# Optimization experiments

Measured on AMD Instinct MI355X. Metric: run time of the kernel, lower is better.

The kernel has to match this reference:

```python
import jax, jax.numpy as jnp
import numpy as np

N_NODES = 50000


def _gin_conv(x, src, dst, w1, b1, w2, b2):
    # sum-aggregate neighbor features: agg[i] = sum_{(j->i) in E} x[j]
    agg = jax.ops.segment_sum(x[src], dst, num_segments=N_NODES)
    h = x + agg  # eps = 0 (PyG GINConv default, not trainable)
    h = jnp.maximum(h @ w1 + b1, 0.0) @ w2 + b2
    return h


def setup_inputs() -> dict:
    key = jax.random.key(0)
    ks = jax.random.split(key, 10)
    d_in, d_h, d_out = 128, 256, 2
    E = 600000
    x = jax.random.normal(ks[0], (N_NODES, d_in), dtype=jnp.float32)
    edge_index = jax.random.randint(ks[1], (2, E), 0, N_NODES, dtype=jnp.int64)
    s = lambda k, sh: jax.random.normal(k, sh, dtype=jnp.float32) * (1.0 / np.sqrt(sh[0]))
    return {
        "x": x,
        "edge_index": edge_index,
        "w1": s(ks[2], (d_in, d_h)), "b1": jnp.zeros((d_h,), jnp.float32),
        "w2": s(ks[3], (d_h, d_h)), "b2": jnp.zeros((d_h,), jnp.float32),
        "w3": s(ks[4], (d_h, d_h)), "b3": jnp.zeros((d_h,), jnp.float32),
        "w4": s(ks[5], (d_h, d_out)), "b4": jnp.zeros((d_out,), jnp.float32),
    }


def reference(x, edge_index, w1, b1, w2, b2, w3, b3, w4, b4):
    src, dst = edge_index[0], edge_index[1]
    h = _gin_conv(x, src, dst, w1, b1, w2, b2)
    h = jnp.maximum(h, 0.0)  # F.relu between the two GINConv layers
    h = _gin_conv(h, src, dst, w3, b3, w4, b4)
    return jax.nn.log_softmax(h, axis=1)
```

## Files before the change

### kernel.cpp

```cpp
#include <hip/hip_runtime.h>
#include <hip/hip_bf16.h>


typedef __attribute__((ext_vector_type(8))) short bf16x8;
typedef __attribute__((ext_vector_type(4))) float f32x4;

static __device__ __forceinline__ unsigned short f2bf(float f) {
    unsigned int u = __float_as_uint(f);
    unsigned int r = (u + 0x7fffu + ((u >> 16) & 1u)) >> 16;
    return (unsigned short)r;
}
static __device__ __forceinline__ float bf2f(unsigned short s) {
    return __uint_as_float(((unsigned int)s) << 16);
}
static __device__ __forceinline__ float bflo(unsigned int u) {
    return __uint_as_float(u << 16);
}
static __device__ __forceinline__ float bfhi(unsigned int u) {
    return __uint_as_float(u & 0xffff0000u);
}

#define S1 136
#define S2 264

__global__ __launch_bounds__(256) void prep_kernel(
    const float* __restrict__ x, short* __restrict__ x_bf,
    const float* __restrict__ w1, const float* __restrict__ w2, const float* __restrict__ w3,
    short* __restrict__ w1t, short* __restrict__ w2t, short* __restrict__ w3t,
    int* __restrict__ deg, int M, int zB, int cB)
{
    const int b = blockIdx.x;
    const int t = threadIdx.x;
    if (b < zB) {
        const int idx = b * 1024 + t * 4;
        if (idx + 3 < M) {
            *(int4*)(deg + idx) = make_int4(0, 0, 0, 0);
        } else {
            #pragma unroll
            for (int i = 0; i < 4; ++i) if (idx + i < M) deg[idx + i] = 0;
        }
        return;
    }
    if (b < zB + cB) {
        const int i = (b - zB) * 256 + t;
        const int n4 = M * 32;
        if (i >= n4) return;
        const float4 v = *(const float4*)(x + (size_t)i * 4);
        ushort4 o;
        o.x = f2bf(v.x); o.y = f2bf(v.y); o.z = f2bf(v.z); o.w = f2bf(v.w);
        *(ushort4*)(x_bf + (size_t)i * 4) = o;
        return;
    }
    const int tb = b - zB - cB;
    const int z = tb >> 6;
    const int rem = tb & 63;
    const int kb = rem & 7;
    const int nb = rem >> 3;
    const float* in; short* outb; int K, ostride;
    if (z == 0)      { in = w1; outb = w1t; K = 128; ostride = S1; }
    else if (z == 1) { in = w2; outb = w2t; K = 256; ostride = S2; }
    else             { in = w3; outb = w3t; K = 256; ostride = S2; }
    const int N = 256;
    const int k0 = kb * 32;
    if (k0 >= K) return;
    const int n0 = nb * 32;
    __shared__ float tile[32][33];
    const int tx = t & 31;
    const int ty = t >> 5;
    #pragma unroll
    for (int i = 0; i < 4; ++i)
        tile[ty + 8 * i][tx] = in[(size_t)(k0 + ty + 8 * i) * N + n0 + tx];
    __syncthreads();
    #pragma unroll
    for (int i = 0; i < 4; ++i)
        outb[(size_t)(n0 + ty + 8 * i) * ostride + k0 + tx] = (short)f2bf(tile[tx][ty + 8 * i]);
}

__global__ __launch_bounds__(256) void degree_kernel(
    const int* __restrict__ dst, int* __restrict__ deg, int E)
{
    const int e = blockIdx.x * 256 + threadIdx.x;
    if (e < E) atomicAdd(&deg[dst[e]], 1);
}

__global__ __launch_bounds__(256) void block_sum_kernel(
    const int* __restrict__ deg, int* __restrict__ bsum, int M)
{
    const int b = blockIdx.x, t = threadIdx.x;
    const int idx = b * 1024 + t * 4;
    int s = 0;
    if (idx + 3 < M) {
        const int4 v = *(const int4*)(deg + idx);
        s = v.x + v.y + v.z + v.w;
    } else {
        #pragma unroll
        for (int i = 0; i < 4; ++i) if (idx + i < M) s += deg[idx + i];
    }
    #pragma unroll
    for (int off = 32; off > 0; off >>= 1) s += __shfl_down(s, off);
    __shared__ int ws[4];
    if ((t & 63) == 0) ws[t >> 6] = s;
    __syncthreads();
    if (t == 0) bsum[b] = ws[0] + ws[1] + ws[2] + ws[3];
}

__global__ __launch_bounds__(256) void scan_blocks2_kernel(
    const int* __restrict__ deg, const int* __restrict__ bsum,
    int* __restrict__ rowptr, int* __restrict__ cur, int M, int E, int nB)
{
    const int b = blockIdx.x, t = threadIdx.x;
    __shared__ int sboff;
    if (t < 64) {
        const int v = (t < nB) ? bsum[t] : 0;
        int inc = v;
        #pragma unroll
        for (int off = 1; off < 64; off <<= 1) {
            const int u = __shfl_up(inc, off);
            if (t >= off) inc += u;
        }
        const int prev = __shfl(inc, (b == 0) ? 0 : (b - 1));
        if (t == 0) sboff = (b == 0) ? 0 : prev;
    }
    const int idx = b * 1024 + t * 4;
    int4 d = make_int4(0, 0, 0, 0);
    if (idx + 3 < M) {
        d = *(const int4*)(deg + idx);
    } else {
        if (idx + 0 < M) d.x = deg[idx + 0];
        if (idx + 1 < M) d.y = deg[idx + 1];
        if (idx + 2 < M) d.z = deg[idx + 2];
        if (idx + 3 < M) d.w = deg[idx + 3];
    }
    const int tot = d.x + d.y + d.z + d.w;
    const int lane = t & 63, wid = t >> 6;
    int inc = tot;
    #pragma unroll
    for (int off = 1; off < 64; off <<= 1) {
        const int u = __shfl_up(inc, off);
        if (lane >= off) inc += u;
    }
    __shared__ int wsum[4];
    if (lane == 63) wsum[wid] = inc;
    __syncthreads();
    int woff = 0;
    #pragma unroll
    for (int w = 0; w < 4; ++w) if (w < wid) woff += wsum[w];
    int p = sboff + woff + (inc - tot);
    if (idx + 0 < M) { rowptr[idx + 0] = p; cur[idx + 0] = p; } p += d.x;
    if (idx + 1 < M) { rowptr[idx + 1] = p; cur[idx + 1] = p; } p += d.y;
    if (idx + 2 < M) { rowptr[idx + 2] = p; cur[idx + 2] = p; } p += d.z;
    if (idx + 3 < M) { rowptr[idx + 3] = p; cur[idx + 3] = p; }
    if (b == 0 && t == 0) rowptr[M] = E;
}

__global__ __launch_bounds__(256) void fill_kernel(
    const int* __restrict__ src, const int* __restrict__ dst,
    int* __restrict__ cur, int* __restrict__ srcs, int E)
{
    const int e = blockIdx.x * 256 + threadIdx.x;
    if (e >= E) return;
    const int p = atomicAdd(&cur[dst[e]], 1);
    srcs[p] = src[e];
}

__global__ __launch_bounds__(256) void gather_add_d128(
    const short* __restrict__ feat,
    const int* __restrict__ rowptr, const int* __restrict__ srcs,
    short* __restrict__ outb, int M)
{
    const int row = blockIdx.x * 4 + (threadIdx.x >> 6);
    if (row >= M) return;
    const int lane = threadIdx.x & 63;
    const int half = lane >> 5;
    const int o = (lane & 31) * 4;
    float a0 = 0.f, a1 = 0.f, a2 = 0.f, a3 = 0.f;
    if (half == 0) {
        const uint2 u = *(const uint2*)(feat + (size_t)row * 128 + o);
        a0 = bflo(u.x); a1 = bfhi(u.x); a2 = bflo(u.y); a3 = bfhi(u.y);
    }
    const int jb = rowptr[row], je = rowptr[row + 1];
    int j = jb;
    for (; j + 8 <= je; j += 8) {
        uint2 v[4];
        #pragma unroll
        for (int t = 0; t < 4; ++t) {
            const int s = srcs[j + 2 * t + half];
            v[t] = *(const uint2*)(feat + (size_t)s * 128 + o);
        }
        #pragma unroll
        for (int t = 0; t < 4; ++t) {
            a0 += bflo(v[t].x); a1 += bfhi(v[t].x);
            a2 += bflo(v[t].y); a3 += bfhi(v[t].y);
        }
    }
    for (; j + 2 <= je; j += 2) {
        const int s = srcs[j + half];
        const uint2 v = *(const uint2*)(feat + (size_t)s * 128 + o);
        a0 += bflo(v.x); a1 += bfhi(v.x); a2 += bflo(v.y); a3 += bfhi(v.y);
    }
    if (j < je && half == 0) {
        const uint2 v = *(const uint2*)(feat + (size_t)srcs[j] * 128 + o);
        a0 += bflo(v.x); a1 += bfhi(v.x); a2 += bflo(v.y); a3 += bfhi(v.y);
    }
    a0 += __shfl_down(a0, 32);
    a1 += __shfl_down(a1, 32);
    a2 += __shfl_down(a2, 32);
    a3 += __shfl_down(a3, 32);
    if (half == 0) {
        uint2 up;
        up.x = (unsigned int)f2bf(a0) | ((unsigned int)f2bf(a1) << 16);
        up.y = (unsigned int)f2bf(a2) | ((unsigned int)f2bf(a3) << 16);
        *(uint2*)(outb + (size_t)row * S1 + o) = up;
    }
}

__global__ __launch_bounds__(256) void gather_add_d256(
    const short* __restrict__ feat,
    const int* __restrict__ rowptr, const int* __restrict__ srcs,
    short* __restrict__ outb, int M)
{
    const int row = blockIdx.x * 4 + (threadIdx.x >> 6);
    if (row >= M) return;
    const int lane = threadIdx.x & 63;
    const int half = lane >> 5;
    const int o = (lane & 31) * 8;
    float a[8];
    #pragma unroll
    for (int k = 0; k < 8; ++k) a[k] = 0.f;
    if (half == 0) {
        const uint4 u = *(const uint4*)(feat + (size_t)row * 256 + o);
        a[0] = bflo(u.x); a[1] = bfhi(u.x); a[2] = bflo(u.y); a[3] = bfhi(u.y);
        a[4] = bflo(u.z); a[5] = bfhi(u.z); a[6] = bflo(u.w); a[7] = bfhi(u.w);
    }
    const int jb = rowptr[row], je = rowptr[row + 1];
    int j = jb;
    for (; j + 8 <= je; j += 8) {
        uint4 v[4];
        #pragma unroll
        for (int t = 0; t < 4; ++t) {
            const int s = srcs[j + 2 * t + half];
            v[t] = *(const uint4*)(feat + (size_t)s * 256 + o);
        }
        #pragma unroll
        for (int t = 0; t < 4; ++t) {
            a[0] += bflo(v[t].x); a[1] += bfhi(v[t].x);
            a[2] += bflo(v[t].y); a[3] += bfhi(v[t].y);
            a[4] += bflo(v[t].z); a[5] += bfhi(v[t].z);
            a[6] += bflo(v[t].w); a[7] += bfhi(v[t].w);
        }
    }
    for (; j + 2 <= je; j += 2) {
        const int s = srcs[j + half];
        const uint4 v = *(const uint4*)(feat + (size_t)s * 256 + o);
        a[0] += bflo(v.x); a[1] += bfhi(v.x); a[2] += bflo(v.y); a[3] += bfhi(v.y);
        a[4] += bflo(v.z); a[5] += bfhi(v.z); a[6] += bflo(v.w); a[7] += bfhi(v.w);
    }
    if (j < je && half == 0) {
        const uint4 v = *(const uint4*)(feat + (size_t)srcs[j] * 256 + o);
        a[0] += bflo(v.x); a[1] += bfhi(v.x); a[2] += bflo(v.y); a[3] += bfhi(v.y);
        a[4] += bflo(v.z); a[5] += bfhi(v.z); a[6] += bflo(v.w); a[7] += bfhi(v.w);
    }
    #pragma unroll
    for (int k = 0; k < 8; ++k) a[k] += __shfl_down(a[k], 32);
    if (half == 0) {
        uint4 up;
        up.x = (unsigned int)f2bf(a[0]) | ((unsigned int)f2bf(a[1]) << 16);
        up.y = (unsigned int)f2bf(a[2]) | ((unsigned int)f2bf(a[3]) << 16);
        up.z = (unsigned int)f2bf(a[4]) | ((unsigned int)f2bf(a[5]) << 16);
        up.w = (unsigned int)f2bf(a[6]) | ((unsigned int)f2bf(a[7]) << 16);
        *(uint4*)(outb + (size_t)row * S2 + o) = up;
    }
}

__global__ __launch_bounds__(256) void layer1_fused(
    const short* __restrict__ h1in,
    const short* __restrict__ w1t,
    const float* __restrict__ b1,
    const short* __restrict__ w2t,
    const float* __restrict__ b2,
    short* __restrict__ h1,
    int M)
{
    __shared__ short sT[64 * S2];
    const int tid  = threadIdx.x;
    const int lane = tid & 63;
    const int wid  = tid >> 6;
    const int r16  = lane & 15;
    const int q    = lane >> 4;
    const int tm   = blockIdx.x * 64;
    const int wn   = wid * 64;

    f32x4 acc[4][4];
    #pragma unroll
    for (int i = 0; i < 4; ++i)
        #pragma unroll
        for (int j = 0; j < 4; ++j)
            acc[i][j] = (f32x4)0.f;

    const short* Abase = h1in + (size_t)tm * S1;
    #pragma unroll
    for (int k0 = 0; k0 < 128; k0 += 32) {
        bf16x8 af[4], bfr[4];
        #pragma unroll
        for (int i = 0; i < 4; ++i)
            af[i] = *(const bf16x8*)(Abase + (size_t)(i * 16 + r16) * S1 + k0 + q * 8);
        #pragma unroll
        for (int j = 0; j < 4; ++j)
            bfr[j] = *(const bf16x8*)(w1t + (size_t)(wn + j * 16 + r16) * S1 + k0 + q * 8);
        #pragma unroll
        for (int i = 0; i < 4; ++i)
            #pragma unroll
            for (int j = 0; j < 4; ++j)
                acc[i][j] = __builtin_amdgcn_mfma_f32_16x16x32_bf16(af[i], bfr[j], acc[i][j], 0, 0, 0);
    }

    #pragma unroll
    for (int j = 0; j < 4; ++j) {
        const int col = wn + j * 16 + r16;
        const float bj = b1[col];
        #pragma unroll
        for (int i = 0; i < 4; ++i)
            #pragma unroll
            for (int r = 0; r < 4; ++r) {
                float v = fmaxf(acc[i][j][r] + bj, 0.f);
                sT[(i * 16 + q * 4 + r) * S2 + col] = (short)f2bf(v);
            }
    }
    __syncthreads();

    #pragma unroll
    for (int i = 0; i < 4; ++i)
        #pragma unroll
        for (int j = 0; j < 4; ++j)
            acc[i][j] = (f32x4)0.f;

    #pragma unroll
    for (int k0 = 0; k0 < 256; k0 += 32) {
        bf16x8 af[4], bfr[4];
        #pragma unroll
        for (int i = 0; i < 4; ++i)
            af[i] = *(const bf16x8*)(&sT[(i * 16 + r16) * S2 + k0 + q * 8]);
        #pragma unroll
        for (int j = 0; j < 4; ++j)
            bfr[j] = *(const bf16x8*)(w2t + (size_t)(wn + j * 16 + r16) * S2 + k0 + q * 8);
        #pragma unroll
        for (int i = 0; i < 4; ++i)
            #pragma unroll
            for (int j = 0; j < 4; ++j)
                acc[i][j] = __builtin_amdgcn_mfma_f32_16x16x32_bf16(af[i], bfr[j], acc[i][j], 0, 0, 0);
    }
    __syncthreads();

    #pragma unroll
    for (int j = 0; j < 4; ++j) {
        const int col = wn + j * 16 + r16;
        const float bj = b2[col];
        #pragma unroll
        for (int i = 0; i < 4; ++i)
            #pragma unroll
            for (int r = 0; r < 4; ++r) {
                float v = fmaxf(acc[i][j][r] + bj, 0.f);
                sT[(i * 16 + q * 4 + r) * S2 + col] = (short)f2bf(v);
            }
    }
    __syncthreads();

    #pragma unroll
    for (int c = 0; c < 8; ++c) {
        const int idx = tid + c * 256;
        const int row = idx >> 5;
        const int ch  = idx & 31;
        const int rg  = tm + row;
        if (rg < M) {
            const uint4 v = *(const uint4*)(&sT[row * S2 + ch * 8]);
            *(uint4*)(h1 + (size_t)rg * 256 + ch * 8) = v;
        }
    }
}

__global__ __launch_bounds__(256) void layer2_fused(
    const short* __restrict__ h2in,
    const short* __restrict__ w3t,
    const float* __restrict__ b3,
    const float* __restrict__ w4,
    const float* __restrict__ b4,
    float* __restrict__ out,
    int M)
{
    __shared__ short sT[64 * S2];
    const int tid  = threadIdx.x;
    const int lane = tid & 63;
    const int wid  = tid >> 6;
    const int r16  = lane & 15;
    const int q    = lane >> 4;
    const int tm   = blockIdx.x * 64;
    const int wn   = wid * 64;

    f32x4 acc[4][4];
    #pragma unroll
    for (int i = 0; i < 4; ++i)
        #pragma unroll
        for (int j = 0; j < 4; ++j)
            acc[i][j] = (f32x4)0.f;

    const short* Abase = h2in + (size_t)tm * S2;
    #pragma unroll
    for (int k0 = 0; k0 < 256; k0 += 32) {
        bf16x8 af[4], bfr[4];
        #pragma unroll
        for (int i = 0; i < 4; ++i)
            af[i] = *(const bf16x8*)(Abase + (size_t)(i * 16 + r16) * S2 + k0 + q * 8);
        #pragma unroll
        for (int j = 0; j < 4; ++j)
            bfr[j] = *(const bf16x8*)(w3t + (size_t)(wn + j * 16 + r16) * S2 + k0 + q * 8);
        #pragma unroll
        for (int i = 0; i < 4; ++i)
            #pragma unroll
            for (int j = 0; j < 4; ++j)
                acc[i][j] = __builtin_amdgcn_mfma_f32_16x16x32_bf16(af[i], bfr[j], acc[i][j], 0, 0, 0);
    }

    #pragma unroll
    for (int j = 0; j < 4; ++j) {
        const int col = wn + j * 16 + r16;
        const float bj = b3[col];
        #pragma unroll
        for (int i = 0; i < 4; ++i)
            #pragma unroll
            for (int r = 0; r < 4; ++r) {
                float v = fmaxf(acc[i][j][r] + bj, 0.f);
                sT[(i * 16 + q * 4 + r) * S2 + col] = (short)f2bf(v);
            }
    }
    __syncthreads();

    const int row = tid >> 2;
    const int qd  = tid & 3;
    const short* tp = &sT[row * S2 + qd * 64];
    const float* w4p = w4 + qd * 128;
    float s0 = 0.f, s1 = 0.f;
    #pragma unroll 8
    for (int k = 0; k < 64; ++k) {
        const float a = bf2f((unsigned short)tp[k]);
        const float2 w = *(const float2*)(w4p + 2 * k);
        s0 = fmaf(a, w.x, s0);
        s1 = fmaf(a, w.y, s1);
    }
    s0 += __shfl_down(s0, 2, 4);  s1 += __shfl_down(s1, 2, 4);
    s0 += __shfl_down(s0, 1, 4);  s1 += __shfl_down(s1, 1, 4);
    if (qd == 0) {
        const int rg = tm + row;
        if (rg < M) {
            s0 += b4[0];
            s1 += b4[1];
            const float m = fmaxf(s0, s1);
            const float l = logf(__expf(s0 - m) + __expf(s1 - m));
            float2 o;
            o.x = s0 - m - l;
            o.y = s1 - m - l;
            *(float2*)(out + (size_t)rg * 2) = o;
        }
    }
}

extern "C" void kernel_launch(void* const* d_in, const int* in_sizes, int n_in,
                              void* d_out, int out_size, void* d_ws, size_t ws_size,
                              hipStream_t stream)
{
    const float* x  = (const float*)d_in[0];
    const int*   ei = (const int*)d_in[1];
    const float* w1 = (const float*)d_in[2];
    const float* b1 = (const float*)d_in[3];
    const float* w2 = (const float*)d_in[4];
    const float* b2 = (const float*)d_in[5];
    const float* w3 = (const float*)d_in[6];
    const float* b3 = (const float*)d_in[7];
    const float* w4 = (const float*)d_in[8];
    const float* b4 = (const float*)d_in[9];

    const int DIN = 128, DH = 256;
    const int M = in_sizes[0] / DIN;
    const int E = in_sizes[1] / 2;
    const int* src = ei;
    const int* dst = ei + E;
    const int nB = (M + 1023) / 1024;

    int* deg    = (int*)d_ws;
    int* cur    = deg + M;
    int* rowptr = cur + M;
    int* bsum   = rowptr + (M + 1);
    int* srcs   = bsum + 64;
    size_t off = ((size_t)(3 * M + 1 + 64 + E) * sizeof(int) + 255) & ~(size_t)255;
    short* x_bf = (short*)((char*)d_ws + off);  off += (size_t)M * DIN * 2;
    off = (off + 255) & ~(size_t)255;
    short* h1in = (short*)((char*)d_ws + off);  off += (size_t)M * S1 * 2;
    off = (off + 255) & ~(size_t)255;
    short* h1   = (short*)((char*)d_ws + off);  off += (size_t)M * DH * 2;
    off = (off + 255) & ~(size_t)255;
    short* h2in = (short*)((char*)d_ws + off);  off += (size_t)M * S2 * 2;
    off = (off + 255) & ~(size_t)255;
    short* w1t  = (short*)((char*)d_ws + off);  off += (size_t)DH * S1 * 2;
    off = (off + 255) & ~(size_t)255;
    short* w2t  = (short*)((char*)d_ws + off);  off += (size_t)DH * S2 * 2;
    off = (off + 255) & ~(size_t)255;
    short* w3t  = (short*)((char*)d_ws + off);  off += (size_t)DH * S2 * 2;

    const int zB = nB;
    const int cB = (M * 32 + 255) / 256;
    prep_kernel<<<zB + cB + 192, 256, 0, stream>>>(
        x, x_bf, w1, w2, w3, w1t, w2t, w3t, deg, M, zB, cB);

    degree_kernel<<<(E + 255) / 256, 256, 0, stream>>>(dst, deg, E);
    block_sum_kernel<<<nB, 256, 0, stream>>>(deg, bsum, M);
    scan_blocks2_kernel<<<nB, 256, 0, stream>>>(deg, bsum, rowptr, cur, M, E, nB);
    fill_kernel<<<(E + 255) / 256, 256, 0, stream>>>(src, dst, cur, srcs, E);

    const int nblk = (M + 63) / 64;

    gather_add_d128<<<(M + 3) / 4, 256, 0, stream>>>(x_bf, rowptr, srcs, h1in, M);
    layer1_fused<<<nblk, 256, 0, stream>>>(h1in, w1t, b1, w2t, b2, h1, M);

    gather_add_d256<<<(M + 3) / 4, 256, 0, stream>>>(h1, rowptr, srcs, h2in, M);
    layer2_fused<<<nblk, 256, 0, stream>>>(h2in, w3t, b3, w4, b4, (float*)d_out, M);
}
```

Before: 285.1 us.

## Fuse neighbor gather-aggregation into MLP kernels and merge degree counting into prep

Each GIN layer's sum-aggregation now writes its result straight into shared memory inside the MLP kernel, with the row tile shrunk to 32 rows. This removes the global h1in/h2in intermediates and two kernel launches. The degree atomics move into the prep kernel, and degree zeroing becomes a hipMemsetAsync. The cost is that each block runs its gather serially, 8 rows per wave, and MFMA work per block is smaller, so latency hiding in the gather and weight reuse in the GEMM may get worse.

```diff
diff --git a/kernel.cpp b/kernel.cpp
--- a/kernel.cpp
+++ b/kernel.cpp
@@ -22,27 +22,19 @@
 
 #define S1 136
 #define S2 264
+#define TM 32
 
 __global__ __launch_bounds__(256) void prep_kernel(
     const float* __restrict__ x, short* __restrict__ x_bf,
     const float* __restrict__ w1, const float* __restrict__ w2, const float* __restrict__ w3,
     short* __restrict__ w1t, short* __restrict__ w2t, short* __restrict__ w3t,
-    int* __restrict__ deg, int M, int zB, int cB)
+    const int* __restrict__ dst, int* __restrict__ deg,
+    int M, int E, int cB)
 {
     const int b = blockIdx.x;
     const int t = threadIdx.x;
-    if (b < zB) {
-        const int idx = b * 1024 + t * 4;
-        if (idx + 3 < M) {
-            *(int4*)(deg + idx) = make_int4(0, 0, 0, 0);
-        } else {
-            #pragma unroll
-            for (int i = 0; i < 4; ++i) if (idx + i < M) deg[idx + i] = 0;
-        }
-        return;
-    }
-    if (b < zB + cB) {
-        const int i = (b - zB) * 256 + t;
+    if (b < cB) {
+        const int i = b * 256 + t;
         const int n4 = M * 32;
         if (i >= n4) return;
         const float4 v = *(const float4*)(x + (size_t)i * 4);
@@ -51,35 +43,33 @@
         *(ushort4*)(x_bf + (size_t)i * 4) = o;
         return;
     }
-    const int tb = b - zB - cB;
-    const int z = tb >> 6;
-    const int rem = tb & 63;
-    const int kb = rem & 7;
-    const int nb = rem >> 3;
-    const float* in; short* outb; int K, ostride;
-    if (z == 0)      { in = w1; outb = w1t; K = 128; ostride = S1; }
-    else if (z == 1) { in = w2; outb = w2t; K = 256; ostride = S2; }
-    else             { in = w3; outb = w3t; K = 256; ostride = S2; }
-    const int N = 256;
-    const int k0 = kb * 32;
-    if (k0 >= K) return;
-    const int n0 = nb * 32;
-    __shared__ float tile[32][33];
-    const int tx = t & 31;
-    const int ty = t >> 5;
-    #pragma unroll
-    for (int i = 0; i < 4; ++i)
-        tile[ty + 8 * i][tx] = in[(size_t)(k0 + ty + 8 * i) * N + n0 + tx];
-    __syncthreads();
-    #pragma unroll
-    for (int i = 0; i < 4; ++i)
-        outb[(size_t)(n0 + ty + 8 * i) * ostride + k0 + tx] = (short)f2bf(tile[tx][ty + 8 * i]);
-}
-
-__global__ __launch_bounds__(256) void degree_kernel(
-    const int* __restrict__ dst, int* __restrict__ deg, int E)
-{
-    const int e = blockIdx.x * 256 + threadIdx.x;
+    if (b < cB + 192) {
+        const int tb = b - cB;
+        const int z = tb >> 6;
+        const int rem = tb & 63;
+        const int kb = rem & 7;
+        const int nb = rem >> 3;
+        const float* in; short* outb; int K, ostride;
+        if (z == 0)      { in = w1; outb = w1t; K = 128; ostride = S1; }
+        else if (z == 1) { in = w2; outb = w2t; K = 256; ostride = S2; }
+        else             { in = w3; outb = w3t; K = 256; ostride = S2; }
+        const int N = 256;
+        const int k0 = kb * 32;
+        if (k0 >= K) return;
+        const int n0 = nb * 32;
+        __shared__ float tile[32][33];
+        const int tx = t & 31;
+        const int ty = t >> 5;
+        #pragma unroll
+        for (int i = 0; i < 4; ++i)
+            tile[ty + 8 * i][tx] = in[(size_t)(k0 + ty + 8 * i) * N + n0 + tx];
+        __syncthreads();
+        #pragma unroll
+        for (int i = 0; i < 4; ++i)
+            outb[(size_t)(n0 + ty + 8 * i) * ostride + k0 + tx] = (short)f2bf(tile[tx][ty + 8 * i]);
+        return;
+    }
+    const int e = (b - cB - 192) * 256 + t;
     if (e < E) atomicAdd(&deg[dst[e]], 1);
 }
 
@@ -163,117 +153,9 @@
     srcs[p] = src[e];
 }
 
-__global__ __launch_bounds__(256) void gather_add_d128(
-    const short* __restrict__ feat,
+__global__ __launch_bounds__(256) void fused_layer1(
+    const short* __restrict__ x_bf,
     const int* __restrict__ rowptr, const int* __restrict__ srcs,
-    short* __restrict__ outb, int M)
-{
-    const int row = blockIdx.x * 4 + (threadIdx.x >> 6);
-    if (row >= M) return;
-    const int lane = threadIdx.x & 63;
-    const int half = lane >> 5;
-    const int o = (lane & 31) * 4;
-    float a0 = 0.f, a1 = 0.f, a2 = 0.f, a3 = 0.f;
-    if (half == 0) {
-        const uint2 u = *(const uint2*)(feat + (size_t)row * 128 + o);
-        a0 = bflo(u.x); a1 = bfhi(u.x); a2 = bflo(u.y); a3 = bfhi(u.y);
-    }
-    const int jb = rowptr[row], je = rowptr[row + 1];
-    int j = jb;
-    for (; j + 8 <= je; j += 8) {
-        uint2 v[4];
-        #pragma unroll
-        for (int t = 0; t < 4; ++t) {
-            const int s = srcs[j + 2 * t + half];
-            v[t] = *(const uint2*)(feat + (size_t)s * 128 + o);
-        }
-        #pragma unroll
-        for (int t = 0; t < 4; ++t) {
-            a0 += bflo(v[t].x); a1 += bfhi(v[t].x);
-            a2 += bflo(v[t].y); a3 += bfhi(v[t].y);
-        }
-    }
-    for (; j + 2 <= je; j += 2) {
-        const int s = srcs[j + half];
-        const uint2 v = *(const uint2*)(feat + (size_t)s * 128 + o);
-        a0 += bflo(v.x); a1 += bfhi(v.x); a2 += bflo(v.y); a3 += bfhi(v.y);
-    }
-    if (j < je && half == 0) {
-        const uint2 v = *(const uint2*)(feat + (size_t)srcs[j] * 128 + o);
-        a0 += bflo(v.x); a1 += bfhi(v.x); a2 += bflo(v.y); a3 += bfhi(v.y);
-    }
-    a0 += __shfl_down(a0, 32);
-    a1 += __shfl_down(a1, 32);
-    a2 += __shfl_down(a2, 32);
-    a3 += __shfl_down(a3, 32);
-    if (half == 0) {
-        uint2 up;
-        up.x = (unsigned int)f2bf(a0) | ((unsigned int)f2bf(a1) << 16);
-        up.y = (unsigned int)f2bf(a2) | ((unsigned int)f2bf(a3) << 16);
-        *(uint2*)(outb + (size_t)row * S1 + o) = up;
-    }
-}
-
-__global__ __launch_bounds__(256) void gather_add_d256(
-    const short* __restrict__ feat,
-    const int* __restrict__ rowptr, const int* __restrict__ srcs,
-    short* __restrict__ outb, int M)
-{
-    const int row = blockIdx.x * 4 + (threadIdx.x >> 6);
-    if (row >= M) return;
-    const int lane = threadIdx.x & 63;
-    const int half = lane >> 5;
-    const int o = (lane & 31) * 8;
-    float a[8];
-    #pragma unroll
-    for (int k = 0; k < 8; ++k) a[k] = 0.f;
-    if (half == 0) {
-        const uint4 u = *(const uint4*)(feat + (size_t)row * 256 + o);
-        a[0] = bflo(u.x); a[1] = bfhi(u.x); a[2] = bflo(u.y); a[3] = bfhi(u.y);
-        a[4] = bflo(u.z); a[5] = bfhi(u.z); a[6] = bflo(u.w); a[7] = bfhi(u.w);
-    }
-    const int jb = rowptr[row], je = rowptr[row + 1];
-    int j = jb;
-    for (; j + 8 <= je; j += 8) {
-        uint4 v[4];
-        #pragma unroll
-        for (int t = 0; t < 4; ++t) {
-            const int s = srcs[j + 2 * t + half];
-            v[t] = *(const uint4*)(feat + (size_t)s * 256 + o);
-        }
-        #pragma unroll
-        for (int t = 0; t < 4; ++t) {
-            a[0] += bflo(v[t].x); a[1] += bfhi(v[t].x);
-            a[2] += bflo(v[t].y); a[3] += bfhi(v[t].y);
-            a[4] += bflo(v[t].z); a[5] += bfhi(v[t].z);
-            a[6] += bflo(v[t].w); a[7] += bfhi(v[t].w);
-        }
-    }
-    for (; j + 2 <= je; j += 2) {
-        const int s = srcs[j + half];
-        const uint4 v = *(const uint4*)(feat + (size_t)s * 256 + o);
-        a[0] += bflo(v.x); a[1] += bfhi(v.x); a[2] += bflo(v.y); a[3] += bfhi(v.y);
-        a[4] += bflo(v.z); a[5] += bfhi(v.z); a[6] += bflo(v.w); a[7] += bfhi(v.w);
-    }
-    if (j < je && half == 0) {
-        const uint4 v = *(const uint4*)(feat + (size_t)srcs[j] * 256 + o);
-        a[0] += bflo(v.x); a[1] += bfhi(v.x); a[2] += bflo(v.y); a[3] += bfhi(v.y);
-        a[4] += bflo(v.z); a[5] += bfhi(v.z); a[6] += bflo(v.w); a[7] += bfhi(v.w);
-    }
-    #pragma unroll
-    for (int k = 0; k < 8; ++k) a[k] += __shfl_down(a[k], 32);
-    if (half == 0) {
-        uint4 up;
-        up.x = (unsigned int)f2bf(a[0]) | ((unsigned int)f2bf(a[1]) << 16);
-        up.y = (unsigned int)f2bf(a[2]) | ((unsigned int)f2bf(a[3]) << 16);
-        up.z = (unsigned int)f2bf(a[4]) | ((unsigned int)f2bf(a[5]) << 16);
-        up.w = (unsigned int)f2bf(a[6]) | ((unsigned int)f2bf(a[7]) << 16);
-        *(uint4*)(outb + (size_t)row * S2 + o) = up;
-    }
-}
-
-__global__ __launch_bounds__(256) void layer1_fused(
-    const short* __restrict__ h1in,
     const short* __restrict__ w1t,
     const float* __restrict__ b1,
     const short* __restrict__ w2t,
@@ -281,70 +163,120 @@
     short* __restrict__ h1,
     int M)
 {
-    __shared__ short sT[64 * S2];
+    __shared__ short sBuf[TM * S2];
     const int tid  = threadIdx.x;
     const int lane = tid & 63;
     const int wid  = tid >> 6;
     const int r16  = lane & 15;
     const int q    = lane >> 4;
-    const int tm   = blockIdx.x * 64;
+    const int tm   = blockIdx.x * TM;
     const int wn   = wid * 64;
 
-    f32x4 acc[4][4];
-    #pragma unroll
-    for (int i = 0; i < 4; ++i)
+    {
+        const int half = lane >> 5;
+        const int o = (lane & 31) * 4;
+        for (int rr = 0; rr < 8; ++rr) {
+            const int r = wid * 8 + rr;
+            const int rg = tm + r;
+            if (rg >= M) break;
+            float a0 = 0.f, a1 = 0.f, a2 = 0.f, a3 = 0.f;
+            if (half == 0) {
+                const uint2 u = *(const uint2*)(x_bf + (size_t)rg * 128 + o);
+                a0 = bflo(u.x); a1 = bfhi(u.x); a2 = bflo(u.y); a3 = bfhi(u.y);
+            }
+            const int jb = rowptr[rg], je = rowptr[rg + 1];
+            int j = jb;
+            for (; j + 8 <= je; j += 8) {
+                uint2 v[4];
+                #pragma unroll
+                for (int t2 = 0; t2 < 4; ++t2) {
+                    const int s = srcs[j + 2 * t2 + half];
+                    v[t2] = *(const uint2*)(x_bf + (size_t)s * 128 + o);
+                }
+                #pragma unroll
+                for (int t2 = 0; t2 < 4; ++t2) {
+                    a0 += bflo(v[t2].x); a1 += bfhi(v[t2].x);
+                    a2 += bflo(v[t2].y); a3 += bfhi(v[t2].y);
+                }
+            }
+            for (; j + 2 <= je; j += 2) {
+                const int s = srcs[j + half];
+                const uint2 v = *(const uint2*)(x_bf + (size_t)s * 128 + o);
+                a0 += bflo(v.x); a1 += bfhi(v.x); a2 += bflo(v.y); a3 += bfhi(v.y);
+            }
+            if (j < je && half == 0) {
+                const uint2 v = *(const uint2*)(x_bf + (size_t)srcs[j] * 128 + o);
+                a0 += bflo(v.x); a1 += bfhi(v.x); a2 += bflo(v.y); a3 += bfhi(v.y);
+            }
+            a0 += __shfl_down(a0, 32);
+            a1 += __shfl_down(a1, 32);
+            a2 += __shfl_down(a2, 32);
+            a3 += __shfl_down(a3, 32);
+            if (half == 0) {
+                uint2 up;
+                up.x = (unsigned int)f2bf(a0) | ((unsigned int)f2bf(a1) << 16);
+                up.y = (unsigned int)f2bf(a2) | ((unsigned int)f2bf(a3) << 16);
+                *(uint2*)(&sBuf[r * S1 + o]) = up;
+            }
+        }
+    }
+    __syncthreads();
+
+    f32x4 acc[2][4];
+    #pragma unroll
+    for (int i = 0; i < 2; ++i)
         #pragma unroll
         for (int j = 0; j < 4; ++j)
             acc[i][j] = (f32x4)0.f;
 
-    const short* Abase = h1in + (size_t)tm * S1;
     #pragma unroll
     for (int k0 = 0; k0 < 128; k0 += 32) {
-        bf16x8 af[4], bfr[4];
-        #pragma unroll
-        for (int i = 0; i < 4; ++i)
-            af[i] = *(const bf16x8*)(Abase + (size_t)(i * 16 + r16) * S1 + k0 + q * 8);
+        bf16x8 af[2], bfr[4];
+        #pragma unroll
+        for (int i = 0; i < 2; ++i)
+            af[i] = *(const bf16x8*)(&sBuf[(i * 16 + r16) * S1 + k0 + q * 8]);
         #pragma unroll
         for (int j = 0; j < 4; ++j)
             bfr[j] = *(const bf16x8*)(w1t + (size_t)(wn + j * 16 + r16) * S1 + k0 + q * 8);
         #pragma unroll
-        for (int i = 0; i < 4; ++i)
+        for (int i = 0; i < 2; ++i)
             #pragma unroll
             for (int j = 0; j < 4; ++j)
                 acc[i][j] = __builtin_amdgcn_mfma_f32_16x16x32_bf16(af[i], bfr[j], acc[i][j], 0, 0, 0);
     }
+    __syncthreads();
 
     #pragma unroll
     for (int j = 0; j < 4; ++j) {
         const int col = wn + j * 16 + r16;
         const float bj = b1[col];
         #pragma unroll
-        for (int i = 0; i < 4; ++i)
+        for (int i = 0; i < 2; ++i)
             #pragma unroll
             for (int r = 0; r < 4; ++r) {
                 float v = fmaxf(acc[i][j][r] + bj, 0.f);
-                sT[(i * 16 + q * 4 + r) * S2 + col] = (short)f2bf(v);
-            }
-    }
-    __syncthreads();
-
-    #pragma unroll
-    for (int i = 0; i < 4; ++i)
+                sBuf[(i * 16 + q * 4 + r) * S2 + col] = (short)f2bf(v);
+            }
+    }
+    __syncthreads();
+
+    #pragma unroll
+    for (int i = 0; i < 2; ++i)
         #pragma unroll
         for (int j = 0; j < 4; ++j)
             acc[i][j] = (f32x4)0.f;
 
     #pragma unroll
     for (int k0 = 0; k0 < 256; k0 += 32) {
-        bf16x8 af[4], bfr[4];
-        #pragma unroll
-        for (int i = 0; i < 4; ++i)
-            af[i] = *(const bf16x8*)(&sT[(i * 16 + r16) * S2 + k0 + q * 8]);
+        bf16x8 af[2], bfr[4];
+        #pragma unroll
+        for (int i = 0; i < 2; ++i)
+            af[i] = *(const bf16x8*)(&sBuf[(i * 16 + r16) * S2 + k0 + q * 8]);
         #pragma unroll
         for (int j = 0; j < 4; ++j)
             bfr[j] = *(const bf16x8*)(w2t + (size_t)(wn + j * 16 + r16) * S2 + k0 + q * 8);
         #pragma unroll
-        for (int i = 0; i < 4; ++i)
+        for (int i = 0; i < 2; ++i)
             #pragma unroll
             for (int j = 0; j < 4; ++j)
                 acc[i][j] = __builtin_amdgcn_mfma_f32_16x16x32_bf16(af[i], bfr[j], acc[i][j], 0, 0, 0);
@@ -356,30 +288,31 @@
         const int col = wn + j * 16 + r16;
         const float bj = b2[col];
         #pragma unroll
-        for (int i = 0; i < 4; ++i)
+        for (int i = 0; i < 2; ++i)
             #pragma unroll
             for (int r = 0; r < 4; ++r) {
                 float v = fmaxf(acc[i][j][r] + bj, 0.f);
-                sT[(i * 16 + q * 4 + r) * S2 + col] = (short)f2bf(v);
-            }
-    }
-    __syncthreads();
-
-    #pragma unroll
-    for (int c = 0; c < 8; ++c) {
+                sBuf[(i * 16 + q * 4 + r) * S2 + col] = (short)f2bf(v);
+            }
+    }
+    __syncthreads();
+
+    #pragma unroll
+    for (int c = 0; c < 4; ++c) {
         const int idx = tid + c * 256;
         const int row = idx >> 5;
         const int ch  = idx & 31;
         const int rg  = tm + row;
         if (rg < M) {
-            const uint4 v = *(const uint4*)(&sT[row * S2 + ch * 8]);
+            const uint4 v = *(const uint4*)(&sBuf[row * S2 + ch * 8]);
             *(uint4*)(h1 + (size_t)rg * 256 + ch * 8) = v;
         }
     }
 }
 
-__global__ __launch_bounds__(256) void layer2_fused(
-    const short* __restrict__ h2in,
+__global__ __launch_bounds__(256) void fused_layer2(
+    const short* __restrict__ h1,
+    const int* __restrict__ rowptr, const int* __restrict__ srcs,
     const short* __restrict__ w3t,
     const float* __restrict__ b3,
     const float* __restrict__ w4,
@@ -387,67 +320,125 @@
     float* __restrict__ out,
     int M)
 {
-    __shared__ short sT[64 * S2];
+    __shared__ short sBuf[TM * S2];
     const int tid  = threadIdx.x;
     const int lane = tid & 63;
     const int wid  = tid >> 6;
     const int r16  = lane & 15;
     const int q    = lane >> 4;
-    const int tm   = blockIdx.x * 64;
+    const int tm   = blockIdx.x * TM;
     const int wn   = wid * 64;
 
-    f32x4 acc[4][4];
-    #pragma unroll
-    for (int i = 0; i < 4; ++i)
+    {
+        const int half = lane >> 5;
+        const int o = (lane & 31) * 8;
+        for (int rr = 0; rr < 8; ++rr) {
+            const int r = wid * 8 + rr;
+            const int rg = tm + r;
+            if (rg >= M) break;
+            float a[8];
+            #pragma unroll
+            for (int k = 0; k < 8; ++k) a[k] = 0.f;
+            if (half == 0) {
+                const uint4 u = *(const uint4*)(h1 + (size_t)rg * 256 + o);
+                a[0] = bflo(u.x); a[1] = bfhi(u.x); a[2] = bflo(u.y); a[3] = bfhi(u.y);
+                a[4] = bflo(u.z); a[5] = bfhi(u.z); a[6] = bflo(u.w); a[7] = bfhi(u.w);
+            }
+            const int jb = rowptr[rg], je = rowptr[rg + 1];
+            int j = jb;
+            for (; j + 8 <= je; j += 8) {
+                uint4 v[4];
+                #pragma unroll
+                for (int t2 = 0; t2 < 4; ++t2) {
+                    const int s = srcs[j + 2 * t2 + half];
+                    v[t2] = *(const uint4*)(h1 + (size_t)s * 256 + o);
+                }
+                #pragma unroll
+                for (int t2 = 0; t2 < 4; ++t2) {
+                    a[0] += bflo(v[t2].x); a[1] += bfhi(v[t2].x);
+                    a[2] += bflo(v[t2].y); a[3] += bfhi(v[t2].y);
+                    a[4] += bflo(v[t2].z); a[5] += bfhi(v[t2].z);
+                    a[6] += bflo(v[t2].w); a[7] += bfhi(v[t2].w);
+                }
+            }
+            for (; j + 2 <= je; j += 2) {
+                const int s = srcs[j + half];
+                const uint4 v = *(const uint4*)(h1 + (size_t)s * 256 + o);
+                a[0] += bflo(v.x); a[1] += bfhi(v.x); a[2] += bflo(v.y); a[3] += bfhi(v.y);
+                a[4] += bflo(v.z); a[5] += bfhi(v.z); a[6] += bflo(v.w); a[7] += bfhi(v.w);
+            }
+            if (j < je && half == 0) {
+                const uint4 v = *(const uint4*)(h1 + (size_t)srcs[j] * 256 + o);
+                a[0] += bflo(v.x); a[1] += bfhi(v.x); a[2] += bflo(v.y); a[3] += bfhi(v.y);
+                a[4] += bflo(v.z); a[5] += bfhi(v.z); a[6] += bflo(v.w); a[7] += bfhi(v.w);
+            }
+            #pragma unroll
+            for (int k = 0; k < 8; ++k) a[k] += __shfl_down(a[k], 32);
+            if (half == 0) {
+                uint4 up;
+                up.x = (unsigned int)f2bf(a[0]) | ((unsigned int)f2bf(a[1]) << 16);
+                up.y = (unsigned int)f2bf(a[2]) | ((unsigned int)f2bf(a[3]) << 16);
+                up.z = (unsigned int)f2bf(a[4]) | ((unsigned int)f2bf(a[5]) << 16);
+                up.w = (unsigned int)f2bf(a[6]) | ((unsigned int)f2bf(a[7]) << 16);
+                *(uint4*)(&sBuf[r * S2 + o]) = up;
+            }
+        }
+    }
+    __syncthreads();
+
+    f32x4 acc[2][4];
+    #pragma unroll
+    for (int i = 0; i < 2; ++i)
         #pragma unroll
         for (int j = 0; j < 4; ++j)
             acc[i][j] = (f32x4)0.f;
 
-    const short* Abase = h2in + (size_t)tm * S2;
     #pragma unroll
     for (int k0 = 0; k0 < 256; k0 += 32) {
-        bf16x8 af[4], bfr[4];
-        #pragma unroll
-        for (int i = 0; i < 4; ++i)
-            af[i] = *(const bf16x8*)(Abase + (size_t)(i * 16 + r16) * S2 + k0 + q * 8);
+        bf16x8 af[2], bfr[4];
+        #pragma unroll
+        for (int i = 0; i < 2; ++i)
+            af[i] = *(const bf16x8*)(&sBuf[(i * 16 + r16) * S2 + k0 + q * 8]);
         #pragma unroll
         for (int j = 0; j < 4; ++j)
             bfr[j] = *(const bf16x8*)(w3t + (size_t)(wn + j * 16 + r16) * S2 + k0 + q * 8);
         #pragma unroll
-        for (int i = 0; i < 4; ++i)
+        for (int i = 0; i < 2; ++i)
             #pragma unroll
             for (int j = 0; j < 4; ++j)
                 acc[i][j] = __builtin_amdgcn_mfma_f32_16x16x32_bf16(af[i], bfr[j], acc[i][j], 0, 0, 0);
     }
+    __syncthreads();
 
     #pragma unroll
     for (int j = 0; j < 4; ++j) {
         const int col = wn + j * 16 + r16;
         const float bj = b3[col];
         #pragma unroll
-        for (int i = 0; i < 4; ++i)
+        for (int i = 0; i < 2; ++i)
             #pragma unroll
             for (int r = 0; r < 4; ++r) {
                 float v = fmaxf(acc[i][j][r] + bj, 0.f);
-                sT[(i * 16 + q * 4 + r) * S2 + col] = (short)f2bf(v);
-            }
-    }
-    __syncthreads();
-
-    const int row = tid >> 2;
-    const int qd  = tid & 3;
-    const short* tp = &sT[row * S2 + qd * 64];
-    const float* w4p = w4 + qd * 128;
+                sBuf[(i * 16 + q * 4 + r) * S2 + col] = (short)f2bf(v);
+            }
+    }
+    __syncthreads();
+
+    const int row = tid >> 3;
+    const int qd  = tid & 7;
+    const short* tp = &sBuf[row * S2 + qd * 32];
+    const float* w4p = w4 + qd * 64;
     float s0 = 0.f, s1 = 0.f;
     #pragma unroll 8
-    for (int k = 0; k < 64; ++k) {
+    for (int k = 0; k < 32; ++k) {
         const float a = bf2f((unsigned short)tp[k]);
         const float2 w = *(const float2*)(w4p + 2 * k);
         s0 = fmaf(a, w.x, s0);
         s1 = fmaf(a, w.y, s1);
     }
-    s0 += __shfl_down(s0, 2, 4);  s1 += __shfl_down(s1, 2, 4);
-    s0 += __shfl_down(s0, 1, 4);  s1 += __shfl_down(s1, 1, 4);
+    s0 += __shfl_down(s0, 4, 8);  s1 += __shfl_down(s1, 4, 8);
+    s0 += __shfl_down(s0, 2, 8);  s1 += __shfl_down(s1, 2, 8);
+    s0 += __shfl_down(s0, 1, 8);  s1 += __shfl_down(s1, 1, 8);
     if (qd == 0) {
         const int rg = tm + row;
         if (rg < M) {
@@ -493,11 +484,7 @@
     size_t off = ((size_t)(3 * M + 1 + 64 + E) * sizeof(int) + 255) & ~(size_t)255;
     short* x_bf = (short*)((char*)d_ws + off);  off += (size_t)M * DIN * 2;
     off = (off + 255) & ~(size_t)255;
-    short* h1in = (short*)((char*)d_ws + off);  off += (size_t)M * S1 * 2;
-    off = (off + 255) & ~(size_t)255;
     short* h1   = (short*)((char*)d_ws + off);  off += (size_t)M * DH * 2;
-    off = (off + 255) & ~(size_t)255;
-    short* h2in = (short*)((char*)d_ws + off);  off += (size_t)M * S2 * 2;
     off = (off + 255) & ~(size_t)255;
     short* w1t  = (short*)((char*)d_ws + off);  off += (size_t)DH * S1 * 2;
     off = (off + 255) & ~(size_t)255;
@@ -505,21 +492,18 @@
     off = (off + 255) & ~(size_t)255;
     short* w3t  = (short*)((char*)d_ws + off);  off += (size_t)DH * S2 * 2;
 
-    const int zB = nB;
+    hipMemsetAsync(deg, 0, (size_t)M * sizeof(int), stream);
     const int cB = (M * 32 + 255) / 256;
-    prep_kernel<<<zB + cB + 192, 256, 0, stream>>>(
-        x, x_bf, w1, w2, w3, w1t, w2t, w3t, deg, M, zB, cB);
-
-    degree_kernel<<<(E + 255) / 256, 256, 0, stream>>>(dst, deg, E);
+    const int dB = (E + 255) / 256;
+    prep_kernel<<<cB + 192 + dB, 256, 0, stream>>>(
+        x, x_bf, w1, w2, w3, w1t, w2t, w3t, dst, deg, M, E, cB);
+
     block_sum_kernel<<<nB, 256, 0, stream>>>(deg, bsum, M);
     scan_blocks2_kernel<<<nB, 256, 0, stream>>>(deg, bsum, rowptr, cur, M, E, nB);
-    fill_kernel<<<(E + 255) / 256, 256, 0, stream>>>(src, dst, cur, srcs, E);
-
-    const int nblk = (M + 63) / 64;
-
-    gather_add_d128<<<(M + 3) / 4, 256, 0, stream>>>(x_bf, rowptr, srcs, h1in, M);
-    layer1_fused<<<nblk, 256, 0, stream>>>(h1in, w1t, b1, w2t, b2, h1, M);
-
-    gather_add_d256<<<(M + 3) / 4, 256, 0, stream>>>(h1, rowptr, srcs, h2in, M);
-    layer2_fused<<<nblk, 256, 0, stream>>>(h2in, w3t, b3, w4, b4, (float*)d_out, M);
-}
+    fill_kernel<<<dB, 256, 0, stream>>>(src, dst, cur, srcs, E);
+
+    const int nblk = (M + TM - 1) / TM;
+
+    fused_layer1<<<nblk, 256, 0, stream>>>(x_bf, rowptr, srcs, w1t, b1, w2t, b2, h1, M);
+    fused_layer2<<<nblk, 256, 0, stream>>>(h1, rowptr, srcs, w3t, b3, w4, b4, (float*)d_out, M);
+}
```

Measured after the change: 319.0 us. 1.12x slower.

## Fuse degree counting and block sums into prep kernel; widen d128 gather loads

Applied to the files above, without the earlier changes.

Zeroing of the degree and block-sum arrays moves to a hipMemsetAsync, and the degree atomics now run inside the prep kernel alongside the bf16 conversion and weight transposes. Each edge also atomically bumps its 1024-node block sum, which removes the separate degree and block_sum launches. The d128 gather now uses 16-byte loads, with four edge quarters per wave reduced by two shuffles. The cost is a second atomic per edge, which contends on only about 49 block counters.

```diff
diff --git a/kernel.cpp b/kernel.cpp
--- a/kernel.cpp
+++ b/kernel.cpp
@@ -27,22 +27,13 @@
     const float* __restrict__ x, short* __restrict__ x_bf,
     const float* __restrict__ w1, const float* __restrict__ w2, const float* __restrict__ w3,
     short* __restrict__ w1t, short* __restrict__ w2t, short* __restrict__ w3t,
-    int* __restrict__ deg, int M, int zB, int cB)
+    const int* __restrict__ dst, int* __restrict__ deg, int* __restrict__ bsum,
+    int M, int E, int cB)
 {
     const int b = blockIdx.x;
     const int t = threadIdx.x;
-    if (b < zB) {
-        const int idx = b * 1024 + t * 4;
-        if (idx + 3 < M) {
-            *(int4*)(deg + idx) = make_int4(0, 0, 0, 0);
-        } else {
-            #pragma unroll
-            for (int i = 0; i < 4; ++i) if (idx + i < M) deg[idx + i] = 0;
-        }
-        return;
-    }
-    if (b < zB + cB) {
-        const int i = (b - zB) * 256 + t;
+    if (b < cB) {
+        const int i = b * 256 + t;
         const int n4 = M * 32;
         if (i >= n4) return;
         const float4 v = *(const float4*)(x + (size_t)i * 4);
@@ -51,57 +42,38 @@
         *(ushort4*)(x_bf + (size_t)i * 4) = o;
         return;
     }
-    const int tb = b - zB - cB;
-    const int z = tb >> 6;
-    const int rem = tb & 63;
-    const int kb = rem & 7;
-    const int nb = rem >> 3;
-    const float* in; short* outb; int K, ostride;
-    if (z == 0)      { in = w1; outb = w1t; K = 128; ostride = S1; }
-    else if (z == 1) { in = w2; outb = w2t; K = 256; ostride = S2; }
-    else             { in = w3; outb = w3t; K = 256; ostride = S2; }
-    const int N = 256;
-    const int k0 = kb * 32;
-    if (k0 >= K) return;
-    const int n0 = nb * 32;
-    __shared__ float tile[32][33];
-    const int tx = t & 31;
-    const int ty = t >> 5;
-    #pragma unroll
-    for (int i = 0; i < 4; ++i)
-        tile[ty + 8 * i][tx] = in[(size_t)(k0 + ty + 8 * i) * N + n0 + tx];
-    __syncthreads();
-    #pragma unroll
-    for (int i = 0; i < 4; ++i)
-        outb[(size_t)(n0 + ty + 8 * i) * ostride + k0 + tx] = (short)f2bf(tile[tx][ty + 8 * i]);
-}
-
-__global__ __launch_bounds__(256) void degree_kernel(
-    const int* __restrict__ dst, int* __restrict__ deg, int E)
-{
-    const int e = blockIdx.x * 256 + threadIdx.x;
-    if (e < E) atomicAdd(&deg[dst[e]], 1);
-}
-
-__global__ __launch_bounds__(256) void block_sum_kernel(
-    const int* __restrict__ deg, int* __restrict__ bsum, int M)
-{
-    const int b = blockIdx.x, t = threadIdx.x;
-    const int idx = b * 1024 + t * 4;
-    int s = 0;
-    if (idx + 3 < M) {
-        const int4 v = *(const int4*)(deg + idx);
-        s = v.x + v.y + v.z + v.w;
-    } else {
-        #pragma unroll
-        for (int i = 0; i < 4; ++i) if (idx + i < M) s += deg[idx + i];
-    }
-    #pragma unroll
-    for (int off = 32; off > 0; off >>= 1) s += __shfl_down(s, off);
-    __shared__ int ws[4];
-    if ((t & 63) == 0) ws[t >> 6] = s;
-    __syncthreads();
-    if (t == 0) bsum[b] = ws[0] + ws[1] + ws[2] + ws[3];
+    if (b < cB + 192) {
+        const int tb = b - cB;
+        const int z = tb >> 6;
+        const int rem = tb & 63;
+        const int kb = rem & 7;
+        const int nb = rem >> 3;
+        const float* in; short* outb; int K, ostride;
+        if (z == 0)      { in = w1; outb = w1t; K = 128; ostride = S1; }
+        else if (z == 1) { in = w2; outb = w2t; K = 256; ostride = S2; }
+        else             { in = w3; outb = w3t; K = 256; ostride = S2; }
+        const int N = 256;
+        const int k0 = kb * 32;
+        if (k0 >= K) return;
+        const int n0 = nb * 32;
+        __shared__ float tile[32][33];
+        const int tx = t & 31;
+        const int ty = t >> 5;
+        #pragma unroll
+        for (int i = 0; i < 4; ++i)
+            tile[ty + 8 * i][tx] = in[(size_t)(k0 + ty + 8 * i) * N + n0 + tx];
+        __syncthreads();
+        #pragma unroll
+        for (int i = 0; i < 4; ++i)
+            outb[(size_t)(n0 + ty + 8 * i) * ostride + k0 + tx] = (short)f2bf(tile[tx][ty + 8 * i]);
+        return;
+    }
+    const int e = (b - cB - 192) * 256 + t;
+    if (e < E) {
+        const int d = dst[e];
+        atomicAdd(&deg[d], 1);
+        atomicAdd(&bsum[d >> 10], 1);
+    }
 }
 
 __global__ __launch_bounds__(256) void scan_blocks2_kernel(
@@ -171,46 +143,58 @@
     const int row = blockIdx.x * 4 + (threadIdx.x >> 6);
     if (row >= M) return;
     const int lane = threadIdx.x & 63;
-    const int half = lane >> 5;
-    const int o = (lane & 31) * 4;
-    float a0 = 0.f, a1 = 0.f, a2 = 0.f, a3 = 0.f;
-    if (half == 0) {
-        const uint2 u = *(const uint2*)(feat + (size_t)row * 128 + o);
-        a0 = bflo(u.x); a1 = bfhi(u.x); a2 = bflo(u.y); a3 = bfhi(u.y);
+    const int qt = lane >> 4;
+    const int o = (lane & 15) * 8;
+    float a[8];
+    #pragma unroll
+    for (int k = 0; k < 8; ++k) a[k] = 0.f;
+    if (qt == 0) {
+        const uint4 u = *(const uint4*)(feat + (size_t)row * 128 + o);
+        a[0] = bflo(u.x); a[1] = bfhi(u.x); a[2] = bflo(u.y); a[3] = bfhi(u.y);
+        a[4] = bflo(u.z); a[5] = bfhi(u.z); a[6] = bflo(u.w); a[7] = bfhi(u.w);
     }
     const int jb = rowptr[row], je = rowptr[row + 1];
     int j = jb;
     for (; j + 8 <= je; j += 8) {
-        uint2 v[4];
-        #pragma unroll
-        for (int t = 0; t < 4; ++t) {
-            const int s = srcs[j + 2 * t + half];
-            v[t] = *(const uint2*)(feat + (size_t)s * 128 + o);
-        }
-        #pragma unroll
-        for (int t = 0; t < 4; ++t) {
-            a0 += bflo(v[t].x); a1 += bfhi(v[t].x);
-            a2 += bflo(v[t].y); a3 += bfhi(v[t].y);
-        }
-    }
-    for (; j + 2 <= je; j += 2) {
-        const int s = srcs[j + half];
-        const uint2 v = *(const uint2*)(feat + (size_t)s * 128 + o);
-        a0 += bflo(v.x); a1 += bfhi(v.x); a2 += bflo(v.y); a3 += bfhi(v.y);
-    }
-    if (j < je && half == 0) {
-        const uint2 v = *(const uint2*)(feat + (size_t)srcs[j] * 128 + o);
-        a0 += bflo(v.x); a1 += bfhi(v.x); a2 += bflo(v.y); a3 += bfhi(v.y);
-    }
-    a0 += __shfl_down(a0, 32);
-    a1 += __shfl_down(a1, 32);
-    a2 += __shfl_down(a2, 32);
-    a3 += __shfl_down(a3, 32);
-    if (half == 0) {
-        uint2 up;
-        up.x = (unsigned int)f2bf(a0) | ((unsigned int)f2bf(a1) << 16);
-        up.y = (unsigned int)f2bf(a2) | ((unsigned int)f2bf(a3) << 16);
-        *(uint2*)(outb + (size_t)row * S1 + o) = up;
+        uint4 v[2];
+        #pragma unroll
+        for (int t = 0; t < 2; ++t) {
+            const int s = srcs[j + 4 * t + qt];
+            v[t] = *(const uint4*)(feat + (size_t)s * 128 + o);
+        }
+        #pragma unroll
+        for (int t = 0; t < 2; ++t) {
+            a[0] += bflo(v[t].x); a[1] += bfhi(v[t].x);
+            a[2] += bflo(v[t].y); a[3] += bfhi(v[t].y);
+            a[4] += bflo(v[t].z); a[5] += bfhi(v[t].z);
+            a[6] += bflo(v[t].w); a[7] += bfhi(v[t].w);
+        }
+    }
+    if (j + 4 <= je) {
+        const int s = srcs[j + qt];
+        const uint4 v = *(const uint4*)(feat + (size_t)s * 128 + o);
+        a[0] += bflo(v.x); a[1] += bfhi(v.x); a[2] += bflo(v.y); a[3] += bfhi(v.y);
+        a[4] += bflo(v.z); a[5] += bfhi(v.z); a[6] += bflo(v.w); a[7] += bfhi(v.w);
+        j += 4;
+    }
+    if (j + qt < je) {
+        const int s = srcs[j + qt];
+        const uint4 v = *(const uint4*)(feat + (size_t)s * 128 + o);
+        a[0] += bflo(v.x); a[1] += bfhi(v.x); a[2] += bflo(v.y); a[3] += bfhi(v.y);
+        a[4] += bflo(v.z); a[5] += bfhi(v.z); a[6] += bflo(v.w); a[7] += bfhi(v.w);
+    }
+    #pragma unroll
+    for (int k = 0; k < 8; ++k) {
+        a[k] += __shfl_down(a[k], 16);
+        a[k] += __shfl_down(a[k], 32);
+    }
+    if (qt == 0) {
+        uint4 up;
+        up.x = (unsigned int)f2bf(a[0]) | ((unsigned int)f2bf(a[1]) << 16);
+        up.y = (unsigned int)f2bf(a[2]) | ((unsigned int)f2bf(a[3]) << 16);
+        up.z = (unsigned int)f2bf(a[4]) | ((unsigned int)f2bf(a[5]) << 16);
+        up.w = (unsigned int)f2bf(a[6]) | ((unsigned int)f2bf(a[7]) << 16);
+        *(uint4*)(outb + (size_t)row * S1 + o) = up;
     }
 }
 
@@ -486,10 +470,10 @@
     const int nB = (M + 1023) / 1024;
 
     int* deg    = (int*)d_ws;
-    int* cur    = deg + M;
+    int* bsum   = deg + M;
+    int* cur    = bsum + 64;
     int* rowptr = cur + M;
-    int* bsum   = rowptr + (M + 1);
-    int* srcs   = bsum + 64;
+    int* srcs   = rowptr + (M + 1);
     size_t off = ((size_t)(3 * M + 1 + 64 + E) * sizeof(int) + 255) & ~(size_t)255;
     short* x_bf = (short*)((char*)d_ws + off);  off += (size_t)M * DIN * 2;
     off = (off + 255) & ~(size_t)255;
@@ -505,15 +489,14 @@
     off = (off + 255) & ~(size_t)255;
     short* w3t  = (short*)((char*)d_ws + off);  off += (size_t)DH * S2 * 2;
 
-    const int zB = nB;
+    hipMemsetAsync(deg, 0, (size_t)(M + 64) * sizeof(int), stream);
     const int cB = (M * 32 + 255) / 256;
-    prep_kernel<<<zB + cB + 192, 256, 0, stream>>>(
-        x, x_bf, w1, w2, w3, w1t, w2t, w3t, deg, M, zB, cB);
-
-    degree_kernel<<<(E + 255) / 256, 256, 0, stream>>>(dst, deg, E);
-    block_sum_kernel<<<nB, 256, 0, stream>>>(deg, bsum, M);
+    const int dB = (E + 255) / 256;
+    prep_kernel<<<cB + 192 + dB, 256, 0, stream>>>(
+        x, x_bf, w1, w2, w3, w1t, w2t, w3t, dst, deg, bsum, M, E, cB);
+
     scan_blocks2_kernel<<<nB, 256, 0, stream>>>(deg, bsum, rowptr, cur, M, E, nB);
-    fill_kernel<<<(E + 255) / 256, 256, 0, stream>>>(src, dst, cur, srcs, E);
+    fill_kernel<<<dB, 256, 0, stream>>>(src, dst, cur, srcs, E);
 
     const int nblk = (M + 63) / 64;
 
```

New measurement: 1.111 ms. 290% more time.
